# Kernel tuning notes

Hardware: AMD Instinct MI355X
Metric: run time of the kernel (lower is better)

## Reference

```python
import jax, jax.numpy as jnp
import numpy as np

N = 50000
E = 800000
DIMS = [128, 256, 64, 256, 128]  # encoder 128->256->64, decoder 64->256->128
NEG_SLOPE = 0.01


def setup_inputs() -> dict:
    key = jax.random.key(0)
    keys = jax.random.split(key, 2 + 3 * 4)
    inp = {
        "x": jax.random.normal(keys[0], (N, DIMS[0]), dtype=jnp.float32),
        "edge_index": jax.random.randint(keys[1], (2, E), 0, N, dtype=jnp.int64),
    }
    for i in range(4):
        d_in, d_out = DIMS[i], DIMS[i + 1]
        s = 1.0 / np.sqrt(d_in)
        inp[f"W_rel{i}"] = jax.random.uniform(keys[2 + 3 * i], (d_out, d_in), jnp.float32, -s, s)
        inp[f"W_root{i}"] = jax.random.uniform(keys[3 + 3 * i], (d_out, d_in), jnp.float32, -s, s)
        inp[f"b{i}"] = jax.random.uniform(keys[4 + 3 * i], (d_out,), jnp.float32, -s, s)
    return inp


def graph_conv(x, edge_index, W_rel, W_root, b):
    # PyG GraphConv: lin_rel(sum_{j->i} x_j) + lin_root(x_i), bias in lin_rel
    src, dst = edge_index[0], edge_index[1]
    agg = jax.ops.segment_sum(x[src], dst, num_segments=N)  # [N, d_in]
    return agg @ W_rel.T + b + x @ W_root.T


def reference(x, edge_index,
              W_rel0, W_root0, b0, W_rel1, W_root1, b1,
              W_rel2, W_root2, b2, W_rel3, W_root3, b3):
    params = [(W_rel0, W_root0, b0), (W_rel1, W_root1, b1),
              (W_rel2, W_root2, b2), (W_rel3, W_root3, b3)]
    h = x
    emb = None
    for i, (Wr, Ws, b) in enumerate(params):
        h = graph_conv(h, edge_index, Wr, Ws, b)
        h = jax.nn.leaky_relu(h, negative_slope=NEG_SLOPE)
        if i == 1:  # end of encoder -> embedding
            emb = h
    return h, emb
```

## Files before the change

### kernel.cpp

```cpp
#include <hip/hip_runtime.h>

#define NNODES 50000
#define NCB 196

typedef __attribute__((ext_vector_type(8))) short bf16x8;
typedef __attribute__((ext_vector_type(4))) float f32x4;

#define AS1 __attribute__((address_space(1)))
#define AS3 __attribute__((address_space(3)))

__device__ inline short f2bf(float f) {
    unsigned u = __float_as_uint(f);
    unsigned r = (u + 0x7FFFu + ((u >> 16) & 1u)) >> 16;
    return (short)r;
}
__device__ inline float bf2f(short s) {
    return __uint_as_float(((unsigned)(unsigned short)s) << 16);
}
__device__ inline float2 bfp2f(int p) {
    float2 f;
    f.x = __uint_as_float((unsigned)p << 16);
    f.y = __uint_as_float((unsigned)p & 0xFFFF0000u);
    return f;
}
__device__ inline void addbf8(float* a, int4 v) {
    float2 l0 = bfp2f(v.x), l1 = bfp2f(v.y), l2 = bfp2f(v.z), l3 = bfp2f(v.w);
    a[0] += l0.x; a[1] += l0.y; a[2] += l1.x; a[3] += l1.y;
    a[4] += l2.x; a[5] += l2.y; a[6] += l3.x; a[7] += l3.y;
}
__device__ inline int pack2(float a, float b) {
    return ((int)(unsigned short)f2bf(a)) | ((int)f2bf(b) << 16);
}

__device__ inline int excl_scan_256(int v, int* lds, int tid) {
    int lane = tid & 63, w = tid >> 6;
    int incl = v;
    #pragma unroll
    for (int off = 1; off < 64; off <<= 1) {
        int t = __shfl_up(incl, off, 64);
        if (lane >= off) incl += t;
    }
    if (lane == 63) lds[w] = incl;
    __syncthreads();
    if (tid == 0) {
        int s = 0;
        #pragma unroll
        for (int i = 0; i < 4; i++) { int t = lds[i]; lds[i] = s; s += t; }
    }
    __syncthreads();
    return incl - v + lds[w];
}

#define PREP_HIST 256
#define PREP_CVTX 6250
#define PREP_CVTW 768
__global__ __launch_bounds__(256) void prep(
    const int* __restrict__ dst, int* __restrict__ histG, int E, int chunk,
    const float* __restrict__ x, short* __restrict__ xbf,
    const float* __restrict__ p0, const float* __restrict__ p1,
    const float* __restrict__ p2, const float* __restrict__ p3,
    const float* __restrict__ p4, const float* __restrict__ p5,
    const float* __restrict__ p6, const float* __restrict__ p7,
    short* __restrict__ wbf)
{
    const int tid = threadIdx.x;
    const int bx  = blockIdx.x;
    if (bx < PREP_HIST) {
        __shared__ int h[NCB];
        for (int i = tid; i < NCB; i += 256) h[i] = 0;
        __syncthreads();
        const int beg = bx * chunk;
        const int end = min(beg + chunk, E);
        for (int e = beg + tid; e < end; e += 256)
            atomicAdd(&h[dst[e] >> 8], 1);
        __syncthreads();
        for (int i = tid; i < NCB; i += 256)
            histG[i * 256 + bx] = h[i];
    } else if (bx < PREP_HIST + PREP_CVTX) {
        const int i = (bx - PREP_HIST) * 256 + tid;
        float4 v = ((const float4*)x)[i];
        short4 s;
        s.x = f2bf(v.x); s.y = f2bf(v.y); s.z = f2bf(v.z); s.w = f2bf(v.w);
        *(short4*)(xbf + (size_t)i * 4) = s;
    } else {
        const int g = (bx - PREP_HIST - PREP_CVTX) * 256 + tid;
        const float* src; int off;
        if      (g <  32768) { src = p0; off = g; }
        else if (g <  65536) { src = p1; off = g -  32768; }
        else if (g <  81920) { src = p2; off = g -  65536; }
        else if (g <  98304) { src = p3; off = g -  81920; }
        else if (g < 114688) { src = p4; off = g -  98304; }
        else if (g < 131072) { src = p5; off = g - 114688; }
        else if (g < 163840) { src = p6; off = g - 131072; }
        else                 { src = p7; off = g - 163840; }
        wbf[g] = f2bf(src[off]);
    }
}

__global__ __launch_bounds__(256) void scan_buckets(
    int* __restrict__ histG, int* __restrict__ btot)
{
    __shared__ int lds[8];
    const int tid = threadIdx.x;
    const int b = blockIdx.x;
    int v = histG[b * 256 + tid];
    int ex = excl_scan_256(v, lds, tid);
    histG[b * 256 + tid] = ex;
    if (tid == 255) btot[b] = ex + v;
}

__global__ __launch_bounds__(256) void scan_bases(
    const int* __restrict__ btot, int* __restrict__ bases, int E)
{
    __shared__ int lds[8];
    const int tid = threadIdx.x;
    int v = (tid < NCB) ? btot[tid] : 0;
    int ex = excl_scan_256(v, lds, tid);
    if (tid <= NCB) bases[tid] = ex;
}

__global__ __launch_bounds__(256) void scatter_coarse(
    const int* __restrict__ src, const int* __restrict__ dst,
    const int* __restrict__ histG, const int* __restrict__ bases,
    int* __restrict__ coarse, int E, int chunk)
{
    __shared__ int pos[NCB];
    const int tid = threadIdx.x;
    const int blk = blockIdx.x;
    for (int i = tid; i < NCB; i += 256)
        pos[i] = bases[i] + histG[i * 256 + blk];
    __syncthreads();
    const int beg = blk * chunk;
    const int end = min(beg + chunk, E);
    for (int e = beg + tid; e < end; e += 256) {
        int d = dst[e];
        int p = atomicAdd(&pos[d >> 8], 1);
        coarse[p] = ((d & 255) << 16) | src[e];
    }
}

__global__ __launch_bounds__(256) void fill_from_coarse(
    const int* __restrict__ bases, const int* __restrict__ coarse,
    int* __restrict__ rowptr, int* __restrict__ col, int N)
{
    __shared__ int hist[256], rp[256], pos[256];
    __shared__ int lds[8];
    const int cb  = blockIdx.x;
    const int tid = threadIdx.x;
    const int n0  = cb << 8;
    const int beg = bases[cb], end = bases[cb + 1];
    hist[tid] = 0; pos[tid] = 0;
    __syncthreads();
    for (int e = beg + tid; e < end; e += 256)
        atomicAdd(&hist[coarse[e] >> 16], 1);
    __syncthreads();
    int ex = excl_scan_256(hist[tid], lds, tid);
    rp[tid] = beg + ex;
    if (n0 + tid <= N) rowptr[n0 + tid] = beg + ex;
    __syncthreads();
    for (int e = beg + tid; e < end; e += 256) {
        int pk = coarse[e];
        int dl = pk >> 16;
        int p = atomicAdd(&pos[dl], 1);
        col[rp[dl] + p] = pk & 0xFFFF;
    }
}

__global__ __launch_bounds__(256) void gather_sum128(
    const short* __restrict__ xbf, const int* __restrict__ rowptr,
    const int* __restrict__ col, short* __restrict__ aggbf, int N)
{
    const int wave = threadIdx.x >> 6;
    const int lane = threadIdx.x & 63;
    const int node = blockIdx.x * 4 + wave;
    if (node >= N) return;
    const int g = lane >> 4;
    const int c = lane & 15;
    const int beg = rowptr[node], end = rowptr[node + 1];
    float acc[8] = {};
    const int last = end - 1;
    for (int e = beg; e < end; e += 32) {
        int idx[8];
        #pragma unroll
        for (int t = 0; t < 8; t++)
            idx[t] = col[min(e + t * 4 + g, last)];
        int4 v[8];
        #pragma unroll
        for (int t = 0; t < 8; t++)
            v[t] = *(const int4*)(xbf + (size_t)idx[t] * 128 + c * 8);
        #pragma unroll
        for (int t = 0; t < 8; t++)
            if (e + t * 4 + g < end) addbf8(acc, v[t]);
    }
    #pragma unroll
    for (int k = 0; k < 8; k++) acc[k] += __shfl_down(acc[k], 32);
    #pragma unroll
    for (int k = 0; k < 8; k++) acc[k] += __shfl_down(acc[k], 16);
    if (g == 0) {
        int4 sv;
        sv.x = pack2(acc[0], acc[1]);
        sv.y = pack2(acc[2], acc[3]);
        sv.z = pack2(acc[4], acc[5]);
        sv.w = pack2(acc[6], acc[7]);
        *(int4*)(aggbf + (size_t)node * 128 + c * 8) = sv;
    }
}

__global__ __launch_bounds__(256) void gather_sum64(
    const short* __restrict__ xbf, const int* __restrict__ rowptr,
    const int* __restrict__ col, short* __restrict__ aggbf, int N)
{
    const int wave = threadIdx.x >> 6;
    const int lane = threadIdx.x & 63;
    const int node = blockIdx.x * 4 + wave;
    if (node >= N) return;
    const int g = lane >> 3;
    const int c = lane & 7;
    const int beg = rowptr[node], end = rowptr[node + 1];
    float acc[8] = {};
    const int last = end - 1;
    for (int e = beg; e < end; e += 32) {
        int idx[4];
        #pragma unroll
        for (int t = 0; t < 4; t++)
            idx[t] = col[min(e + t * 8 + g, last)];
        int4 v[4];
        #pragma unroll
        for (int t = 0; t < 4; t++)
            v[t] = *(const int4*)(xbf + (size_t)idx[t] * 64 + c * 8);
        #pragma unroll
        for (int t = 0; t < 4; t++)
            if (e + t * 8 + g < end) addbf8(acc, v[t]);
    }
    #pragma unroll
    for (int k = 0; k < 8; k++) acc[k] += __shfl_down(acc[k], 32);
    #pragma unroll
    for (int k = 0; k < 8; k++) acc[k] += __shfl_down(acc[k], 16);
    #pragma unroll
    for (int k = 0; k < 8; k++) acc[k] += __shfl_down(acc[k], 8);
    if (g == 0) {
        int4 sv;
        sv.x = pack2(acc[0], acc[1]);
        sv.y = pack2(acc[2], acc[3]);
        sv.z = pack2(acc[4], acc[5]);
        sv.w = pack2(acc[6], acc[7]);
        *(int4*)(aggbf + (size_t)node * 64 + c * 8) = sv;
    }
}

__global__ __launch_bounds__(256) void gather_fin128(
    const short* __restrict__ zw, const int* __restrict__ rowptr,
    const int* __restrict__ col, const float* __restrict__ bias,
    float* __restrict__ out, int N)
{
    const int wave = threadIdx.x >> 6;
    const int lane = threadIdx.x & 63;
    const int node = blockIdx.x * 4 + wave;
    if (node >= N) return;
    const int g = lane >> 4;
    const int c = lane & 15;
    const int beg = rowptr[node], end = rowptr[node + 1];
    float acc[8] = {};
    if (g == 0) {
        int4 wv = *(const int4*)(zw + (size_t)node * 256 + 128 + c * 8);
        addbf8(acc, wv);
        float4 b0 = *(const float4*)(bias + c * 8);
        float4 b1 = *(const float4*)(bias + c * 8 + 4);
        acc[0] += b0.x; acc[1] += b0.y; acc[2] += b0.z; acc[3] += b0.w;
        acc[4] += b1.x; acc[5] += b1.y; acc[6] += b1.z; acc[7] += b1.w;
    }
    const int last = end - 1;
    for (int e = beg; e < end; e += 32) {
        int idx[8];
        #pragma unroll
        for (int t = 0; t < 8; t++)
            idx[t] = col[min(e + t * 4 + g, last)];
        int4 v[8];
        #pragma unroll
        for (int t = 0; t < 8; t++)
            v[t] = *(const int4*)(zw + (size_t)idx[t] * 256 + c * 8);
        #pragma unroll
        for (int t = 0; t < 8; t++)
            if (e + t * 4 + g < end) addbf8(acc, v[t]);
    }
    #pragma unroll
    for (int k = 0; k < 8; k++) acc[k] += __shfl_down(acc[k], 32);
    #pragma unroll
    for (int k = 0; k < 8; k++) acc[k] += __shfl_down(acc[k], 16);
    if (g == 0) {
        #pragma unroll
        for (int k = 0; k < 8; k++) acc[k] = acc[k] > 0.f ? acc[k] : 0.01f * acc[k];
        float4 o0 = make_float4(acc[0], acc[1], acc[2], acc[3]);
        float4 o1 = make_float4(acc[4], acc[5], acc[6], acc[7]);
        *(float4*)(out + (size_t)node * 128 + c * 8)     = o0;
        *(float4*)(out + (size_t)node * 128 + c * 8 + 4) = o1;
    }
}

__global__ __launch_bounds__(256) void gather_fin64(
    const short* __restrict__ zw, const int* __restrict__ rowptr,
    const int* __restrict__ col, const float* __restrict__ bias,
    float* __restrict__ out, short* __restrict__ out_bf, int N)
{
    const int wave = threadIdx.x >> 6;
    const int lane = threadIdx.x & 63;
    const int node = blockIdx.x * 4 + wave;
    if (node >= N) return;
    const int g = lane >> 3;
    const int c = lane & 7;
    const int beg = rowptr[node], end = rowptr[node + 1];
    float acc[8] = {};
    if (g == 0) {
        int4 wv = *(const int4*)(zw + (size_t)node * 128 + 64 + c * 8);
        addbf8(acc, wv);
        float4 b0 = *(const float4*)(bias + c * 8);
        float4 b1 = *(const float4*)(bias + c * 8 + 4);
        acc[0] += b0.x; acc[1] += b0.y; acc[2] += b0.z; acc[3] += b0.w;
        acc[4] += b1.x; acc[5] += b1.y; acc[6] += b1.z; acc[7] += b1.w;
    }
    const int last = end - 1;
    for (int e = beg; e < end; e += 32) {
        int idx[4];
        #pragma unroll
        for (int t = 0; t < 4; t++)
            idx[t] = col[min(e + t * 8 + g, last)];
        int4 v[4];
        #pragma unroll
        for (int t = 0; t < 4; t++)
            v[t] = *(const int4*)(zw + (size_t)idx[t] * 128 + c * 8);
        #pragma unroll
        for (int t = 0; t < 4; t++)
            if (e + t * 8 + g < end) addbf8(acc, v[t]);
    }
    #pragma unroll
    for (int k = 0; k < 8; k++) acc[k] += __shfl_down(acc[k], 32);
    #pragma unroll
    for (int k = 0; k < 8; k++) acc[k] += __shfl_down(acc[k], 16);
    #pragma unroll
    for (int k = 0; k < 8; k++) acc[k] += __shfl_down(acc[k], 8);
    if (g == 0) {
        #pragma unroll
        for (int k = 0; k < 8; k++) acc[k] = acc[k] > 0.f ? acc[k] : 0.01f * acc[k];
        float4 o0 = make_float4(acc[0], acc[1], acc[2], acc[3]);
        float4 o1 = make_float4(acc[4], acc[5], acc[6], acc[7]);
        *(float4*)(out + (size_t)node * 64 + c * 8)     = o0;
        *(float4*)(out + (size_t)node * 64 + c * 8 + 4) = o1;
        int4 sv;
        sv.x = pack2(acc[0], acc[1]);
        sv.y = pack2(acc[2], acc[3]);
        sv.z = pack2(acc[4], acc[5]);
        sv.w = pack2(acc[6], acc[7]);
        *(int4*)(out_bf + (size_t)node * 64 + c * 8) = sv;
    }
}

template<int DK, int DOUT, bool FUSED, bool PAIRED>
__global__ __launch_bounds__(512, 2) void gemm_mfma(
    const short* __restrict__ A0, const short* __restrict__ A1,
    const short* __restrict__ B0, const short* __restrict__ B1,
    const float* __restrict__ bias, short* __restrict__ outH, int N)
{
    constexpr int KTOT  = FUSED ? 2 * DK : DK;
    constexpr int NCOLS = FUSED ? DOUT : 2 * DOUT;
    constexpr int K32   = KTOT / 32;
    constexpr int LOG2K32 = (K32 == 8) ? 3 : 2;
    constexpr int BSH   = 128 * KTOT;
    constexpr int BI4   = BSH / 8;
    constexpr int ITER  = BI4 / 512;
    constexpr int EPSH  = 8 * 4608;
    constexpr int SMSH  = (BSH > EPSH) ? BSH : EPSH;
    constexpr int NPAIR = (NNODES + 255) / 256;

    int bx, by;
    if (PAIRED) {
        const int d  = blockIdx.x;
        const int hi = d >> 4, rem = d & 15;
        const int q  = hi * 8 + (rem & 7);
        if (q >= NPAIR) return;
        bx = q; by = rem >> 3;
    } else {
        bx = blockIdx.x; by = 0;
    }

    __shared__ short smem[SMSH];
    const int tid  = threadIdx.x;
    const int row0 = bx * 256;
    const int col0 = by * 128;
    const int w    = tid >> 6;
    const int lane = tid & 63;
    const int wr   = (w & 3) << 6;
    const int wc   = (w >> 2) << 6;
    const int m16  = lane & 15;
    const int quad = lane >> 4;

    #pragma unroll
    for (int it = 0; it < ITER; it++) {
        const int L  = tid + it * 512;
        const int mm = L & 15;
        const int qd = (L >> 4) & 3;
        const int kk = (L >> 6) & (K32 - 1);
        const int jj = L >> (6 + LOG2K32);
        const int j  = col0 + jj * 16 + mm;
        const int ko = (kk * 4 + qd) * 8;
        const short* bp;
        if (FUSED) {
            if (ko < DK) bp = B0 + (size_t)j * DK + ko;
            else         bp = B1 + (size_t)j * DK + (ko - DK);
        } else {
            bp = (j < DOUT) ? (B0 + (size_t)j * DK + ko)
                            : (B1 + (size_t)(j - DOUT) * DK + ko);
        }
        __builtin_amdgcn_global_load_lds(
            (const AS1 void*)bp, (AS3 void*)(smem + ((size_t)L << 3)), 16, 0, 0);
    }
    __syncthreads();

    const short* arow[4];
    #pragma unroll
    for (int i = 0; i < 4; i++) {
        int r = row0 + wr + i * 16 + m16;
        r = r < N ? r : N - 1;
        arow[i] = A0 + (size_t)r * DK + (quad << 3);
    }
    const size_t a1d = FUSED ? (size_t)(A1 - A0) : 0;

    f32x4 acc[4][4] = {};
    const int jw = wc >> 4;

    #pragma unroll
    for (int kk = 0; kk < K32; kk++) {
        const int ko = kk * 32;
        bf16x8 af[4];
        #pragma unroll
        for (int i = 0; i < 4; i++) {
            const short* ap = arow[i];
            if (FUSED && ko >= DK) ap += a1d + (ko - DK);
            else                   ap += ko;
            af[i] = *(const bf16x8*)ap;
        }
        #pragma unroll
        for (int j = 0; j < 4; j++) {
            bf16x8 bfr = *(const bf16x8*)(smem +
                (((((jw + j) * K32 + kk) * 4 + quad) * 16 + m16) << 3));
            #pragma unroll
            for (int i = 0; i < 4; i++)
                acc[i][j] = __builtin_amdgcn_mfma_f32_16x16x32_bf16(
                    bfr, af[i], acc[i][j], 0, 0, 0);
        }
    }

    __syncthreads();

    short* ep = smem + w * 4608;
    #pragma unroll
    for (int j = 0; j < 4; j++) {
        const int cb = wc + j * 16 + (quad << 2);
        float4 bv = make_float4(0.f, 0.f, 0.f, 0.f);
        if (FUSED) bv = *(const float4*)(bias + col0 + cb);
        #pragma unroll
        for (int i = 0; i < 4; i++) {
            float v0 = acc[i][j][0], v1 = acc[i][j][1];
            float v2 = acc[i][j][2], v3 = acc[i][j][3];
            if (FUSED) {
                v0 += bv.x; v1 += bv.y; v2 += bv.z; v3 += bv.w;
                v0 = v0 > 0.f ? v0 : 0.01f * v0;
                v1 = v1 > 0.f ? v1 : 0.01f * v1;
                v2 = v2 > 0.f ? v2 : 0.01f * v2;
                v3 = v3 > 0.f ? v3 : 0.01f * v3;
            }
            int2 pv;
            pv.x = pack2(v0, v1);
            pv.y = pack2(v2, v3);
            *(int2*)(ep + (i * 16 + m16) * 72 + j * 16 + (quad << 2)) = pv;
        }
    }
    const int r8  = lane >> 3;
    const int seg = lane & 7;
    #pragma unroll
    for (int rb = 0; rb < 8; rb++) {
        const int lrow = rb * 8 + r8;
        int4 vv = *(const int4*)(ep + lrow * 72 + seg * 8);
        const int grow = row0 + wr + lrow;
        if (grow < N)
            *(int4*)(outH + (size_t)grow * NCOLS + col0 + wc + seg * 8) = vv;
    }
}

extern "C" void kernel_launch(void* const* d_in, const int* in_sizes, int n_in,
                              void* d_out, int out_size, void* d_ws, size_t ws_size,
                              hipStream_t stream) {
    const int N = NNODES;
    const float* x  = (const float*)d_in[0];
    const int*   ei = (const int*)d_in[1];
    const int    E  = in_sizes[1] / 2;
    const int* src = ei;
    const int* dst = ei + E;

    const float* Wr[4] = { (const float*)d_in[2], (const float*)d_in[5],
                           (const float*)d_in[8], (const float*)d_in[11] };
    const float* Ws[4] = { (const float*)d_in[3], (const float*)d_in[6],
                           (const float*)d_in[9], (const float*)d_in[12] };
    const float* bb[4] = { (const float*)d_in[4], (const float*)d_in[7],
                           (const float*)d_in[10], (const float*)d_in[13] };

    float* out  = (float*)d_out;
    float* emb  = out + (size_t)N * 128;

    short* zwbf   = (short*)d_ws;
    short* aggbf  = zwbf + (size_t)N * 256;
    short* xbf    = aggbf + (size_t)N * 128;
    short* h1bf   = xbf + (size_t)N * 128;
    short* embbf  = h1bf + (size_t)N * 256;
    short* wbf    = embbf + (size_t)N * 64;
    int*   rowptr = (int*)(wbf + 196608);
    int*   col    = rowptr + (N + 1);
    int*   coarse = col + E;
    int*   histG  = coarse + E;
    int*   btot   = histG + NCB * 256;
    int*   bases  = btot + NCB;

    const short* wr0 = wbf;           const short* ws0 = wbf + 32768;
    const short* wr1 = wbf + 65536;   const short* ws1 = wbf + 81920;
    const short* wr2 = wbf + 98304;   const short* ws2 = wbf + 114688;
    const short* wr3 = wbf + 131072;  const short* ws3 = wbf + 163840;

    const int chunk = (E + 255) / 256;
    const int gemmRB = (N + 255) / 256;
    const int pairGrid = ((gemmRB + 7) / 8) * 16;
    const int nodeBlocks = (N + 3) / 4;

    prep<<<PREP_HIST + PREP_CVTX + PREP_CVTW, 256, 0, stream>>>(
        dst, histG, E, chunk, x, xbf,
        Wr[0], Ws[0], Wr[1], Ws[1], Wr[2], Ws[2], Wr[3], Ws[3], wbf);
    scan_buckets<<<NCB, 256, 0, stream>>>(histG, btot);
    scan_bases<<<1, 256, 0, stream>>>(btot, bases, E);
    scatter_coarse<<<256, 256, 0, stream>>>(src, dst, histG, bases, coarse, E, chunk);
    fill_from_coarse<<<NCB, 256, 0, stream>>>(bases, coarse, rowptr, col, N);

    gather_sum128<<<nodeBlocks, 256, 0, stream>>>(xbf, rowptr, col, aggbf, N);
    gemm_mfma<128, 256, true, true><<<pairGrid, 512, 0, stream>>>(
        aggbf, xbf, wr0, ws0, bb[0], h1bf, N);

    gemm_mfma<256, 64, false, false><<<gemmRB, 512, 0, stream>>>(
        h1bf, nullptr, wr1, ws1, nullptr, zwbf, N);
    gather_fin64<<<nodeBlocks, 256, 0, stream>>>(
        zwbf, rowptr, col, bb[1], emb, embbf, N);

    gather_sum64<<<nodeBlocks, 256, 0, stream>>>(embbf, rowptr, col, aggbf, N);
    gemm_mfma<64, 256, true, true><<<pairGrid, 512, 0, stream>>>(
        aggbf, embbf, wr2, ws2, bb[2], h1bf , N);

    gemm_mfma<256, 128, false, true><<<pairGrid, 512, 0, stream>>>(
        h1bf , nullptr, wr3, ws3, nullptr, zwbf, N);
    gather_fin128<<<nodeBlocks, 256, 0, stream>>>(
        zwbf, rowptr, col, bb[3], out, N);
}
```

Before: 308.6 us.

## Fold base scan into scatter/fill, grid-stride gathers, smaller GEMM tile for layer 1

Removes the single-block scan_bases launch by having every scatter_coarse and fill_from_coarse block redundantly rescan the 196 bucket totals in shared memory. The four gather kernels become grid-stride loops over a fixed 3125-block grid, so each wave handles several nodes instead of one block per four nodes. The GEMM template gains a row-tile parameter, and the 256->64 layer now runs with 128-row tiles and 256 threads to get more blocks. These save one launch and some block-scheduling overhead, at the cost of redundant scan work and possibly less latency hiding in the gathers.

```diff
diff --git a/kernel.cpp b/kernel.cpp
--- a/kernel.cpp
+++ b/kernel.cpp
@@ -109,26 +109,22 @@
     if (tid == 255) btot[b] = ex + v;
 }
 
-__global__ __launch_bounds__(256) void scan_bases(
-    const int* __restrict__ btot, int* __restrict__ bases, int E)
-{
+__global__ __launch_bounds__(256) void scatter_coarse(
+    const int* __restrict__ src, const int* __restrict__ dst,
+    const int* __restrict__ histG, const int* __restrict__ btot,
+    int* __restrict__ coarse, int E, int chunk)
+{
+    __shared__ int pos[NCB];
+    __shared__ int sbase[256];
     __shared__ int lds[8];
     const int tid = threadIdx.x;
-    int v = (tid < NCB) ? btot[tid] : 0;
-    int ex = excl_scan_256(v, lds, tid);
-    if (tid <= NCB) bases[tid] = ex;
-}
-
-__global__ __launch_bounds__(256) void scatter_coarse(
-    const int* __restrict__ src, const int* __restrict__ dst,
-    const int* __restrict__ histG, const int* __restrict__ bases,
-    int* __restrict__ coarse, int E, int chunk)
-{
-    __shared__ int pos[NCB];
-    const int tid = threadIdx.x;
     const int blk = blockIdx.x;
+    int bv = (tid < NCB) ? btot[tid] : 0;
+    int bex = excl_scan_256(bv, lds, tid);
+    sbase[tid] = bex;
+    __syncthreads();
     for (int i = tid; i < NCB; i += 256)
-        pos[i] = bases[i] + histG[i * 256 + blk];
+        pos[i] = sbase[i] + histG[i * 256 + blk];
     __syncthreads();
     const int beg = blk * chunk;
     const int end = min(beg + chunk, E);
@@ -140,15 +136,20 @@
 }
 
 __global__ __launch_bounds__(256) void fill_from_coarse(
-    const int* __restrict__ bases, const int* __restrict__ coarse,
+    const int* __restrict__ btot, const int* __restrict__ coarse,
     int* __restrict__ rowptr, int* __restrict__ col, int N)
 {
     __shared__ int hist[256], rp[256], pos[256];
     __shared__ int lds[8];
+    __shared__ int sb[2];
     const int cb  = blockIdx.x;
     const int tid = threadIdx.x;
     const int n0  = cb << 8;
-    const int beg = bases[cb], end = bases[cb + 1];
+    int bv = (tid < NCB) ? btot[tid] : 0;
+    int bex = excl_scan_256(bv, lds, tid);
+    if (tid == cb) { sb[0] = bex; sb[1] = bex + bv; }
+    __syncthreads();
+    const int beg = sb[0], end = sb[1];
     hist[tid] = 0; pos[tid] = 0;
     __syncthreads();
     for (int e = beg + tid; e < end; e += 256)
@@ -172,37 +173,38 @@
 {
     const int wave = threadIdx.x >> 6;
     const int lane = threadIdx.x & 63;
-    const int node = blockIdx.x * 4 + wave;
-    if (node >= N) return;
     const int g = lane >> 4;
     const int c = lane & 15;
-    const int beg = rowptr[node], end = rowptr[node + 1];
-    float acc[8] = {};
-    const int last = end - 1;
-    for (int e = beg; e < end; e += 32) {
-        int idx[8];
-        #pragma unroll
-        for (int t = 0; t < 8; t++)
-            idx[t] = col[min(e + t * 4 + g, last)];
-        int4 v[8];
-        #pragma unroll
-        for (int t = 0; t < 8; t++)
-            v[t] = *(const int4*)(xbf + (size_t)idx[t] * 128 + c * 8);
-        #pragma unroll
-        for (int t = 0; t < 8; t++)
-            if (e + t * 4 + g < end) addbf8(acc, v[t]);
-    }
-    #pragma unroll
-    for (int k = 0; k < 8; k++) acc[k] += __shfl_down(acc[k], 32);
-    #pragma unroll
-    for (int k = 0; k < 8; k++) acc[k] += __shfl_down(acc[k], 16);
-    if (g == 0) {
-        int4 sv;
-        sv.x = pack2(acc[0], acc[1]);
-        sv.y = pack2(acc[2], acc[3]);
-        sv.z = pack2(acc[4], acc[5]);
-        sv.w = pack2(acc[6], acc[7]);
-        *(int4*)(aggbf + (size_t)node * 128 + c * 8) = sv;
+    const int stride = gridDim.x * 4;
+    for (int node = blockIdx.x * 4 + wave; node < N; node += stride) {
+        const int beg = rowptr[node], end = rowptr[node + 1];
+        float acc[8] = {};
+        const int last = end - 1;
+        for (int e = beg; e < end; e += 32) {
+            int idx[8];
+            #pragma unroll
+            for (int t = 0; t < 8; t++)
+                idx[t] = col[min(e + t * 4 + g, last)];
+            int4 v[8];
+            #pragma unroll
+            for (int t = 0; t < 8; t++)
+                v[t] = *(const int4*)(xbf + (size_t)idx[t] * 128 + c * 8);
+            #pragma unroll
+            for (int t = 0; t < 8; t++)
+                if (e + t * 4 + g < end) addbf8(acc, v[t]);
+        }
+        #pragma unroll
+        for (int k = 0; k < 8; k++) acc[k] += __shfl_down(acc[k], 32);
+        #pragma unroll
+        for (int k = 0; k < 8; k++) acc[k] += __shfl_down(acc[k], 16);
+        if (g == 0) {
+            int4 sv;
+            sv.x = pack2(acc[0], acc[1]);
+            sv.y = pack2(acc[2], acc[3]);
+            sv.z = pack2(acc[4], acc[5]);
+            sv.w = pack2(acc[6], acc[7]);
+            *(int4*)(aggbf + (size_t)node * 128 + c * 8) = sv;
+        }
     }
 }
 
@@ -212,39 +214,40 @@
 {
     const int wave = threadIdx.x >> 6;
     const int lane = threadIdx.x & 63;
-    const int node = blockIdx.x * 4 + wave;
-    if (node >= N) return;
     const int g = lane >> 3;
     const int c = lane & 7;
-    const int beg = rowptr[node], end = rowptr[node + 1];
-    float acc[8] = {};
-    const int last = end - 1;
-    for (int e = beg; e < end; e += 32) {
-        int idx[4];
-        #pragma unroll
-        for (int t = 0; t < 4; t++)
-            idx[t] = col[min(e + t * 8 + g, last)];
-        int4 v[4];
-        #pragma unroll
-        for (int t = 0; t < 4; t++)
-            v[t] = *(const int4*)(xbf + (size_t)idx[t] * 64 + c * 8);
-        #pragma unroll
-        for (int t = 0; t < 4; t++)
-            if (e + t * 8 + g < end) addbf8(acc, v[t]);
-    }
-    #pragma unroll
-    for (int k = 0; k < 8; k++) acc[k] += __shfl_down(acc[k], 32);
-    #pragma unroll
-    for (int k = 0; k < 8; k++) acc[k] += __shfl_down(acc[k], 16);
-    #pragma unroll
-    for (int k = 0; k < 8; k++) acc[k] += __shfl_down(acc[k], 8);
-    if (g == 0) {
-        int4 sv;
-        sv.x = pack2(acc[0], acc[1]);
-        sv.y = pack2(acc[2], acc[3]);
-        sv.z = pack2(acc[4], acc[5]);
-        sv.w = pack2(acc[6], acc[7]);
-        *(int4*)(aggbf + (size_t)node * 64 + c * 8) = sv;
+    const int stride = gridDim.x * 4;
+    for (int node = blockIdx.x * 4 + wave; node < N; node += stride) {
+        const int beg = rowptr[node], end = rowptr[node + 1];
+        float acc[8] = {};
+        const int last = end - 1;
+        for (int e = beg; e < end; e += 32) {
+            int idx[4];
+            #pragma unroll
+            for (int t = 0; t < 4; t++)
+                idx[t] = col[min(e + t * 8 + g, last)];
+            int4 v[4];
+            #pragma unroll
+            for (int t = 0; t < 4; t++)
+                v[t] = *(const int4*)(xbf + (size_t)idx[t] * 64 + c * 8);
+            #pragma unroll
+            for (int t = 0; t < 4; t++)
+                if (e + t * 8 + g < end) addbf8(acc, v[t]);
+        }
+        #pragma unroll
+        for (int k = 0; k < 8; k++) acc[k] += __shfl_down(acc[k], 32);
+        #pragma unroll
+        for (int k = 0; k < 8; k++) acc[k] += __shfl_down(acc[k], 16);
+        #pragma unroll
+        for (int k = 0; k < 8; k++) acc[k] += __shfl_down(acc[k], 8);
+        if (g == 0) {
+            int4 sv;
+            sv.x = pack2(acc[0], acc[1]);
+            sv.y = pack2(acc[2], acc[3]);
+            sv.z = pack2(acc[4], acc[5]);
+            sv.w = pack2(acc[6], acc[7]);
+            *(int4*)(aggbf + (size_t)node * 64 + c * 8) = sv;
+        }
     }
 }
 
@@ -255,45 +258,46 @@
 {
     const int wave = threadIdx.x >> 6;
     const int lane = threadIdx.x & 63;
-    const int node = blockIdx.x * 4 + wave;
-    if (node >= N) return;
     const int g = lane >> 4;
     const int c = lane & 15;
-    const int beg = rowptr[node], end = rowptr[node + 1];
-    float acc[8] = {};
-    if (g == 0) {
-        int4 wv = *(const int4*)(zw + (size_t)node * 256 + 128 + c * 8);
-        addbf8(acc, wv);
-        float4 b0 = *(const float4*)(bias + c * 8);
-        float4 b1 = *(const float4*)(bias + c * 8 + 4);
-        acc[0] += b0.x; acc[1] += b0.y; acc[2] += b0.z; acc[3] += b0.w;
-        acc[4] += b1.x; acc[5] += b1.y; acc[6] += b1.z; acc[7] += b1.w;
-    }
-    const int last = end - 1;
-    for (int e = beg; e < end; e += 32) {
-        int idx[8];
-        #pragma unroll
-        for (int t = 0; t < 8; t++)
-            idx[t] = col[min(e + t * 4 + g, last)];
-        int4 v[8];
-        #pragma unroll
-        for (int t = 0; t < 8; t++)
-            v[t] = *(const int4*)(zw + (size_t)idx[t] * 256 + c * 8);
-        #pragma unroll
-        for (int t = 0; t < 8; t++)
-            if (e + t * 4 + g < end) addbf8(acc, v[t]);
-    }
-    #pragma unroll
-    for (int k = 0; k < 8; k++) acc[k] += __shfl_down(acc[k], 32);
-    #pragma unroll
-    for (int k = 0; k < 8; k++) acc[k] += __shfl_down(acc[k], 16);
-    if (g == 0) {
-        #pragma unroll
-        for (int k = 0; k < 8; k++) acc[k] = acc[k] > 0.f ? acc[k] : 0.01f * acc[k];
-        float4 o0 = make_float4(acc[0], acc[1], acc[2], acc[3]);
-        float4 o1 = make_float4(acc[4], acc[5], acc[6], acc[7]);
-        *(float4*)(out + (size_t)node * 128 + c * 8)     = o0;
-        *(float4*)(out + (size_t)node * 128 + c * 8 + 4) = o1;
+    const int stride = gridDim.x * 4;
+    for (int node = blockIdx.x * 4 + wave; node < N; node += stride) {
+        const int beg = rowptr[node], end = rowptr[node + 1];
+        float acc[8] = {};
+        if (g == 0) {
+            int4 wv = *(const int4*)(zw + (size_t)node * 256 + 128 + c * 8);
+            addbf8(acc, wv);
+            float4 b0 = *(const float4*)(bias + c * 8);
+            float4 b1 = *(const float4*)(bias + c * 8 + 4);
+            acc[0] += b0.x; acc[1] += b0.y; acc[2] += b0.z; acc[3] += b0.w;
+            acc[4] += b1.x; acc[5] += b1.y; acc[6] += b1.z; acc[7] += b1.w;
+        }
+        const int last = end - 1;
+        for (int e = beg; e < end; e += 32) {
+            int idx[8];
+            #pragma unroll
+            for (int t = 0; t < 8; t++)
+                idx[t] = col[min(e + t * 4 + g, last)];
+            int4 v[8];
+            #pragma unroll
+            for (int t = 0; t < 8; t++)
+                v[t] = *(const int4*)(zw + (size_t)idx[t] * 256 + c * 8);
+            #pragma unroll
+            for (int t = 0; t < 8; t++)
+                if (e + t * 4 + g < end) addbf8(acc, v[t]);
+        }
+        #pragma unroll
+        for (int k = 0; k < 8; k++) acc[k] += __shfl_down(acc[k], 32);
+        #pragma unroll
+        for (int k = 0; k < 8; k++) acc[k] += __shfl_down(acc[k], 16);
+        if (g == 0) {
+            #pragma unroll
+            for (int k = 0; k < 8; k++) acc[k] = acc[k] > 0.f ? acc[k] : 0.01f * acc[k];
+            float4 o0 = make_float4(acc[0], acc[1], acc[2], acc[3]);
+            float4 o1 = make_float4(acc[4], acc[5], acc[6], acc[7]);
+            *(float4*)(out + (size_t)node * 128 + c * 8)     = o0;
+            *(float4*)(out + (size_t)node * 128 + c * 8 + 4) = o1;
+        }
     }
 }
 
@@ -304,58 +308,59 @@
 {
     const int wave = threadIdx.x >> 6;
     const int lane = threadIdx.x & 63;
-    const int node = blockIdx.x * 4 + wave;
-    if (node >= N) return;
     const int g = lane >> 3;
     const int c = lane & 7;
-    const int beg = rowptr[node], end = rowptr[node + 1];
-    float acc[8] = {};
-    if (g == 0) {
-        int4 wv = *(const int4*)(zw + (size_t)node * 128 + 64 + c * 8);
-        addbf8(acc, wv);
-        float4 b0 = *(const float4*)(bias + c * 8);
-        float4 b1 = *(const float4*)(bias + c * 8 + 4);
-        acc[0] += b0.x; acc[1] += b0.y; acc[2] += b0.z; acc[3] += b0.w;
-        acc[4] += b1.x; acc[5] += b1.y; acc[6] += b1.z; acc[7] += b1.w;
-    }
-    const int last = end - 1;
-    for (int e = beg; e < end; e += 32) {
-        int idx[4];
-        #pragma unroll
-        for (int t = 0; t < 4; t++)
-            idx[t] = col[min(e + t * 8 + g, last)];
-        int4 v[4];
-        #pragma unroll
-        for (int t = 0; t < 4; t++)
-            v[t] = *(const int4*)(zw + (size_t)idx[t] * 128 + c * 8);
-        #pragma unroll
-        for (int t = 0; t < 4; t++)
-            if (e + t * 8 + g < end) addbf8(acc, v[t]);
-    }
-    #pragma unroll
-    for (int k = 0; k < 8; k++) acc[k] += __shfl_down(acc[k], 32);
-    #pragma unroll
-    for (int k = 0; k < 8; k++) acc[k] += __shfl_down(acc[k], 16);
-    #pragma unroll
-    for (int k = 0; k < 8; k++) acc[k] += __shfl_down(acc[k], 8);
-    if (g == 0) {
-        #pragma unroll
-        for (int k = 0; k < 8; k++) acc[k] = acc[k] > 0.f ? acc[k] : 0.01f * acc[k];
-        float4 o0 = make_float4(acc[0], acc[1], acc[2], acc[3]);
-        float4 o1 = make_float4(acc[4], acc[5], acc[6], acc[7]);
-        *(float4*)(out + (size_t)node * 64 + c * 8)     = o0;
-        *(float4*)(out + (size_t)node * 64 + c * 8 + 4) = o1;
-        int4 sv;
-        sv.x = pack2(acc[0], acc[1]);
-        sv.y = pack2(acc[2], acc[3]);
-        sv.z = pack2(acc[4], acc[5]);
-        sv.w = pack2(acc[6], acc[7]);
-        *(int4*)(out_bf + (size_t)node * 64 + c * 8) = sv;
-    }
-}
-
-template<int DK, int DOUT, bool FUSED, bool PAIRED>
-__global__ __launch_bounds__(512, 2) void gemm_mfma(
+    const int stride = gridDim.x * 4;
+    for (int node = blockIdx.x * 4 + wave; node < N; node += stride) {
+        const int beg = rowptr[node], end = rowptr[node + 1];
+        float acc[8] = {};
+        if (g == 0) {
+            int4 wv = *(const int4*)(zw + (size_t)node * 128 + 64 + c * 8);
+            addbf8(acc, wv);
+            float4 b0 = *(const float4*)(bias + c * 8);
+            float4 b1 = *(const float4*)(bias + c * 8 + 4);
+            acc[0] += b0.x; acc[1] += b0.y; acc[2] += b0.z; acc[3] += b0.w;
+            acc[4] += b1.x; acc[5] += b1.y; acc[6] += b1.z; acc[7] += b1.w;
+        }
+        const int last = end - 1;
+        for (int e = beg; e < end; e += 32) {
+            int idx[4];
+            #pragma unroll
+            for (int t = 0; t < 4; t++)
+                idx[t] = col[min(e + t * 8 + g, last)];
+            int4 v[4];
+            #pragma unroll
+            for (int t = 0; t < 4; t++)
+                v[t] = *(const int4*)(zw + (size_t)idx[t] * 128 + c * 8);
+            #pragma unroll
+            for (int t = 0; t < 4; t++)
+                if (e + t * 8 + g < end) addbf8(acc, v[t]);
+        }
+        #pragma unroll
+        for (int k = 0; k < 8; k++) acc[k] += __shfl_down(acc[k], 32);
+        #pragma unroll
+        for (int k = 0; k < 8; k++) acc[k] += __shfl_down(acc[k], 16);
+        #pragma unroll
+        for (int k = 0; k < 8; k++) acc[k] += __shfl_down(acc[k], 8);
+        if (g == 0) {
+            #pragma unroll
+            for (int k = 0; k < 8; k++) acc[k] = acc[k] > 0.f ? acc[k] : 0.01f * acc[k];
+            float4 o0 = make_float4(acc[0], acc[1], acc[2], acc[3]);
+            float4 o1 = make_float4(acc[4], acc[5], acc[6], acc[7]);
+            *(float4*)(out + (size_t)node * 64 + c * 8)     = o0;
+            *(float4*)(out + (size_t)node * 64 + c * 8 + 4) = o1;
+            int4 sv;
+            sv.x = pack2(acc[0], acc[1]);
+            sv.y = pack2(acc[2], acc[3]);
+            sv.z = pack2(acc[4], acc[5]);
+            sv.w = pack2(acc[6], acc[7]);
+            *(int4*)(out_bf + (size_t)node * 64 + c * 8) = sv;
+        }
+    }
+}
+
+template<int DK, int DOUT, bool FUSED, bool PAIRED, int TR>
+__global__ __launch_bounds__(TR * 2, 2) void gemm_mfma(
     const short* __restrict__ A0, const short* __restrict__ A1,
     const short* __restrict__ B0, const short* __restrict__ B1,
     const float* __restrict__ bias, short* __restrict__ outH, int N)
@@ -364,19 +369,22 @@
     constexpr int NCOLS = FUSED ? DOUT : 2 * DOUT;
     constexpr int K32   = KTOT / 32;
     constexpr int LOG2K32 = (K32 == 8) ? 3 : 2;
+    constexpr int NT    = TR * 2;
+    constexpr int NW    = NT / 64;
+    constexpr int RW    = TR / 64;
     constexpr int BSH   = 128 * KTOT;
     constexpr int BI4   = BSH / 8;
-    constexpr int ITER  = BI4 / 512;
-    constexpr int EPSH  = 8 * 4608;
+    constexpr int ITER  = BI4 / NT;
+    constexpr int EPSH  = NW * 4608;
     constexpr int SMSH  = (BSH > EPSH) ? BSH : EPSH;
-    constexpr int NPAIR = (NNODES + 255) / 256;
+    constexpr int NTILE = (NNODES + TR - 1) / TR;
 
     int bx, by;
     if (PAIRED) {
         const int d  = blockIdx.x;
         const int hi = d >> 4, rem = d & 15;
         const int q  = hi * 8 + (rem & 7);
-        if (q >= NPAIR) return;
+        if (q >= NTILE) return;
         bx = q; by = rem >> 3;
     } else {
         bx = blockIdx.x; by = 0;
@@ -384,18 +392,18 @@
 
     __shared__ short smem[SMSH];
     const int tid  = threadIdx.x;
-    const int row0 = bx * 256;
+    const int row0 = bx * TR;
     const int col0 = by * 128;
     const int w    = tid >> 6;
     const int lane = tid & 63;
-    const int wr   = (w & 3) << 6;
-    const int wc   = (w >> 2) << 6;
+    const int wr   = (w & (RW - 1)) << 6;
+    const int wc   = (w / RW) << 6;
     const int m16  = lane & 15;
     const int quad = lane >> 4;
 
     #pragma unroll
     for (int it = 0; it < ITER; it++) {
-        const int L  = tid + it * 512;
+        const int L  = tid + it * NT;
         const int mm = L & 15;
         const int qd = (L >> 4) & 3;
         const int kk = (L >> 6) & (K32 - 1);
@@ -517,7 +525,6 @@
     int*   coarse = col + E;
     int*   histG  = coarse + E;
     int*   btot   = histG + NCB * 256;
-    int*   bases  = btot + NCB;
 
     const short* wr0 = wbf;           const short* ws0 = wbf + 32768;
     const short* wr1 = wbf + 65536;   const short* ws1 = wbf + 81920;
@@ -526,32 +533,32 @@
 
     const int chunk = (E + 255) / 256;
     const int gemmRB = (N + 255) / 256;
+    const int gemmRB128 = (N + 127) / 128;
     const int pairGrid = ((gemmRB + 7) / 8) * 16;
-    const int nodeBlocks = (N + 3) / 4;
+    const int gatherBlocks = 3125;
 
     prep<<<PREP_HIST + PREP_CVTX + PREP_CVTW, 256, 0, stream>>>(
         dst, histG, E, chunk, x, xbf,
         Wr[0], Ws[0], Wr[1], Ws[1], Wr[2], Ws[2], Wr[3], Ws[3], wbf);
     scan_buckets<<<NCB, 256, 0, stream>>>(histG, btot);
-    scan_bases<<<1, 256, 0, stream>>>(btot, bases, E);
-    scatter_coarse<<<256, 256, 0, stream>>>(src, dst, histG, bases, coarse, E, chunk);
-    fill_from_coarse<<<NCB, 256, 0, stream>>>(bases, coarse, rowptr, col, N);
-
-    gather_sum128<<<nodeBlocks, 256, 0, stream>>>(xbf, rowptr, col, aggbf, N);
-    gemm_mfma<128, 256, true, true><<<pairGrid, 512, 0, stream>>>(
+    scatter_coarse<<<256, 256, 0, stream>>>(src, dst, histG, btot, coarse, E, chunk);
+    fill_from_coarse<<<NCB, 256, 0, stream>>>(btot, coarse, rowptr, col, N);
+
+    gather_sum128<<<gatherBlocks, 256, 0, stream>>>(xbf, rowptr, col, aggbf, N);
+    gemm_mfma<128, 256, true, true, 256><<<pairGrid, 512, 0, stream>>>(
         aggbf, xbf, wr0, ws0, bb[0], h1bf, N);
 
-    gemm_mfma<256, 64, false, false><<<gemmRB, 512, 0, stream>>>(
+    gemm_mfma<256, 64, false, false, 128><<<gemmRB128, 256, 0, stream>>>(
         h1bf, nullptr, wr1, ws1, nullptr, zwbf, N);
-    gather_fin64<<<nodeBlocks, 256, 0, stream>>>(
+    gather_fin64<<<gatherBlocks, 256, 0, stream>>>(
         zwbf, rowptr, col, bb[1], emb, embbf, N);
 
-    gather_sum64<<<nodeBlocks, 256, 0, stream>>>(embbf, rowptr, col, aggbf, N);
-    gemm_mfma<64, 256, true, true><<<pairGrid, 512, 0, stream>>>(
+    gather_sum64<<<gatherBlocks, 256, 0, stream>>>(embbf, rowptr, col, aggbf, N);
+    gemm_mfma<64, 256, true, true, 256><<<pairGrid, 512, 0, stream>>>(
         aggbf, embbf, wr2, ws2, bb[2], h1bf , N);
 
-    gemm_mfma<256, 128, false, true><<<pairGrid, 512, 0, stream>>>(
+    gemm_mfma<256, 128, false, true, 256><<<pairGrid, 512, 0, stream>>>(
         h1bf , nullptr, wr3, ws3, nullptr, zwbf, N);
-    gather_fin128<<<nodeBlocks, 256, 0, stream>>>(
+    gather_fin128<<<gatherBlocks, 256, 0, stream>>>(
         zwbf, rowptr, col, bb[3], out, N);
 }
```

Result: slower. 322.3 us (+4.4%).
